# Kernel optimization log

Hardware: AMD Instinct MI355X
Metric: run time of the kernel (lower is better)

Reference implementation:

```python
import jax, jax.numpy as jnp
import numpy as np

T = 10          # time_steps
IN_DIM = 784    # 28*28
HID = 256
NCLS = 47
THRESH = 1.0
TAU_MEM = 2.0   # LIF membrane time constant
TAU_OUT = 2.0   # readout EMA time constant


@jax.custom_vjp
def spike_fn(u):
    # Heaviside spike on (v - threshold), surrogate gradient in bwd.
    return (u >= 0.0).astype(u.dtype)

def _spike_fwd(u):
    return spike_fn(u), u

def _spike_bwd(u, g):
    # sigmoid surrogate derivative, slope 4
    s = jax.nn.sigmoid(4.0 * u)
    return (g * 4.0 * s * (1.0 - s),)

spike_fn.defvjp(_spike_fwd, _spike_bwd)


def setup_inputs() -> dict:
    key = jax.random.key(0)
    k1, k2, k3 = jax.random.split(key, 3)
    x = jax.random.uniform(k1, (4096, 1, 28, 28), dtype=jnp.float32)
    W1 = jax.random.normal(k2, (IN_DIM, HID), dtype=jnp.float32) / np.float32(np.sqrt(IN_DIM))
    b1 = jnp.zeros((HID,), jnp.float32)
    Wr = jax.random.normal(k3, (HID, NCLS), dtype=jnp.float32) / np.float32(np.sqrt(HID))
    br = jnp.zeros((NCLS,), jnp.float32)
    return {"x": x, "W1": W1, "b1": b1, "Wr": Wr, "br": br}


def reference(x, W1, b1, Wr, br):
    B = x.shape[0]
    xf = x.reshape(B, -1)  # [B, 784] pixel intensities in [0,1]
    # rate_encode_flat: Bernoulli(p=pixel) spikes per timestep -> [T, B, 784]
    ek = jax.random.key(42)
    seq = (jax.random.uniform(ek, (T, B, IN_DIM), dtype=xf.dtype) < xf[None]).astype(xf.dtype)

    def step(carry, s_t):
        v_hid, v_out = carry
        I_hid = s_t @ W1 + b1                      # [B, HID]
        v_hid = v_hid + (I_hid - v_hid) / TAU_MEM  # leaky integration
        spk = spike_fn(v_hid - THRESH)             # spike emission
        v_hid = v_hid * (1.0 - spk)                # hard reset to 0
        I = spk @ Wr + br                          # [B, NCLS]
        v_out = v_out + (I - v_out) / TAU_OUT      # output EMA
        return (v_hid, v_out), None

    init = (jnp.zeros((B, HID), xf.dtype), jnp.zeros((B, NCLS), xf.dtype))
    (_, v_out), _ = jax.lax.scan(step, init, seq)
    return v_out
```

## Files before the change

### kernel.cpp

```cpp
#include <hip/hip_runtime.h>
#include <stdint.h>


#define T_STEPS 10
#define BATCH   4096
#define IN_DIM  784
#define HID     256
#define NCLS    47
#define NROWS   (T_STEPS * BATCH)
#define KWORDS  25
#define KPAD    800
#define M_TILE  160

#define WS_W1HI_OFF 46039040u
#define WS_W1MD_OFF (46039040u + 409600u)
#define WS_W1LO_OFF (46039040u + 819200u)

typedef __attribute__((ext_vector_type(8))) short    bf16x8;
typedef __attribute__((ext_vector_type(4))) float    f32x4;
typedef __attribute__((ext_vector_type(4))) uint32_t u32x4;

__device__ __forceinline__ uint32_t rotl32(uint32_t x, uint32_t r) {
    return __builtin_amdgcn_alignbit(x, x, 32u - r);
}

__device__ __forceinline__ uint32_t tf_hash(uint32_t lo) {
    const uint32_t ks1 = 42u;
    const uint32_t ks2 = 0x1BD11BDAu ^ 42u;
    uint32_t x0 = 0u;
    uint32_t x1 = lo + ks1;
#define TF_RND(r) { x0 += x1; x1 = rotl32(x1, r); x1 ^= x0; }
    TF_RND(13) TF_RND(15) TF_RND(26) TF_RND(6)
    x0 += ks1; x1 += ks2 + 1u;
    TF_RND(17) TF_RND(29) TF_RND(16) TF_RND(24)
    x0 += ks2; x1 += 2u;
    TF_RND(13) TF_RND(15) TF_RND(26) TF_RND(6)
    x1 += ks1 + 3u;
    TF_RND(17) TF_RND(29) TF_RND(16) TF_RND(24)
    x0 += ks1; x1 += ks2 + 4u;
    TF_RND(13) TF_RND(15) TF_RND(26) TF_RND(6)
    x0 += ks2; x1 += 5u;
#undef TF_RND
    return x0 ^ x1;
}

__device__ __forceinline__ uint32_t hash2(uint32_t ib, const float* xp) {
    float2 xx = *(const float2*)xp;
    uint32_t w = 0u;
    w |= ((float)(tf_hash(ib + 0u) >> 9) < xx.x * 8388608.0f) ? 0x3F80u : 0u;
    w |= ((float)(tf_hash(ib + 1u) >> 9) < xx.y * 8388608.0f) ? 0x3F800000u : 0u;
    return w;
}

__global__ __launch_bounds__(256) void splitk_k(
        const float* __restrict__ W1, ushort* __restrict__ hiT,
        ushort* __restrict__ midT, ushort* __restrict__ loT) {
    int n = blockIdx.x;
    for (int k = threadIdx.x; k < KPAD; k += 256) {
        float w = (k < IN_DIM) ? W1[k * HID + n] : 0.0f;
        uint32_t u = __float_as_uint(w);
        uint32_t hb = (u + 0x7FFFu + ((u >> 16) & 1u)) >> 16;
        float hf = __uint_as_float(hb << 16);
        float r1 = w - hf;
        uint32_t u1 = __float_as_uint(r1);
        uint32_t mb = (u1 + 0x7FFFu + ((u1 >> 16) & 1u)) >> 16;
        float mf2 = __uint_as_float(mb << 16);
        float r2 = r1 - mf2;
        uint32_t u2 = __float_as_uint(r2);
        uint32_t lb = (u2 + 0x7FFFu + ((u2 >> 16) & 1u)) >> 16;
        hiT [n * KPAD + k] = (ushort)hb;
        midT[n * KPAD + k] = (ushort)mb;
        loT [n * KPAD + k] = (ushort)lb;
    }
}

#define LDS_B0  20480
#define B_BUFSZ 49152
#define A_BUFSZ 10240
#define I0_LDW  258
#define G_LDW   260
#define G_OFF   83200

__global__ __launch_bounds__(512, 1) void fused_gemm_k(
        const ushort* __restrict__ hiT, const ushort* __restrict__ midT,
        const ushort* __restrict__ loT, const float* __restrict__ b1,
        const float* __restrict__ x, const float* __restrict__ Wr,
        const float* __restrict__ br, float* __restrict__ out) {
    __shared__ __align__(16) char lds[118784];

    const int tid = threadIdx.x;
    const int l   = tid & 63;
    const int wv  = tid >> 6;
    const int wm  = wv >> 2;
    const int wn  = wv & 3;
    const int b0  = blockIdx.x << 4;

    f32x4 acc[5][4] = {};

    const int q   = l >> 4;
    const int sig = q ^ (l & 3) ^ ((l >> 2) & 3);
    const int a_rd = wm * 5120 + ((l & 15) << 6) + (sig << 4);
    const int b_rd = (((wn << 6) + (l & 15)) << 6) + (sig << 4);

    const ushort* hi_p[2];
    const ushort* md_p[2];
    const ushort* lo_p[2];
    int bdst[2];
#pragma unroll
    for (int i = 0; i < 2; ++i) {
        int s  = (i << 9) + tid;
        int n  = s >> 2;
        int qs = s & 3;
        int qd = qs ^ (n & 3) ^ ((n >> 2) & 3);
        size_t eoff = (size_t)n * KPAD + ((size_t)qd << 3);
        hi_p[i] = hiT  + eoff;
        md_p[i] = midT + eoff;
        lo_p[i] = loT  + eoff;
        bdst[i] = ((i << 9) + (wv << 6)) << 4;
    }

    int      adst[5];
    const float* txp[5];
    uint32_t tib[5];
    int      tpp[5];
#pragma unroll
    for (int s = 0; s < 5; ++s) {
        int tau = tid + (s << 9);
        int row = tau >> 4;
        int p   = tau & 15;
        int qd  = (p >> 2) ^ (row & 3) ^ ((row >> 2) & 3);
        adst[s] = (row << 6) + (qd << 4) + ((p & 3) << 2);
        int rowg = ((row >> 4) * BATCH) + b0 + (row & 15);
        txp[s]  = x + (size_t)(b0 + (row & 15)) * IN_DIM + (p << 1);
        tib[s]  = (uint32_t)rowg * (uint32_t)IN_DIM + (uint32_t)(p << 1);
        tpp[s]  = p;
    }

#define STAGE_B(koff, bbase) \
    _Pragma("unroll") \
    for (int i = 0; i < 2; ++i) { \
        __builtin_amdgcn_global_load_lds( \
            (const __attribute__((address_space(1))) void*)(hi_p[i] + (koff)), \
            (__attribute__((address_space(3))) void*)(lds + (bbase) + bdst[i]), \
            16, 0, 0); \
        __builtin_amdgcn_global_load_lds( \
            (const __attribute__((address_space(1))) void*)(md_p[i] + (koff)), \
            (__attribute__((address_space(3))) void*)(lds + (bbase) + 16384 + bdst[i]), \
            16, 0, 0); \
        __builtin_amdgcn_global_load_lds( \
            (const __attribute__((address_space(1))) void*)(lo_p[i] + (koff)), \
            (__attribute__((address_space(3))) void*)(lds + (bbase) + 32768 + bdst[i]), \
            16, 0, 0); \
    }

#define HASH_TASK(s, koff, abase, is_tail) { \
    uint32_t w_ = 0u; \
    if (!(is_tail) || tpp[s] < 8) \
        w_ = hash2(tib[s] + (uint32_t)(koff), txp[s] + (koff)); \
    *(uint32_t*)(lds + (abase) + adst[s]) = w_; }

#define MFMA_CHUNK(s) \
    _Pragma("unroll") \
    for (int m = (s) * 12; m < (s) * 12 + 12; ++m) { \
        const int nt_ = m / 15, r_ = m % 15, pl_ = r_ / 5, mt_ = r_ % 5; \
        acc[mt_][nt_] = __builtin_amdgcn_mfma_f32_16x16x32_bf16( \
            af[mt_], bfr[pl_][nt_], acc[mt_][nt_], 0, 0, 0); \
    }

#define PRELOAD_FRAGS(bufidx) \
    const char* A = lds + (bufidx) * A_BUFSZ; \
    const char* B = lds + LDS_B0 + (bufidx) * B_BUFSZ; \
    bf16x8 af[5]; \
    bf16x8 bfr[3][4]; \
    _Pragma("unroll") \
    for (int mt = 0; mt < 5; ++mt) \
        af[mt] = *(const bf16x8*)(A + a_rd + (mt << 10)); \
    _Pragma("unroll") \
    for (int nt = 0; nt < 4; ++nt) { \
        bfr[0][nt] = *(const bf16x8*)(B + b_rd + (nt << 10)); \
        bfr[1][nt] = *(const bf16x8*)(B + 16384 + b_rd + (nt << 10)); \
        bfr[2][nt] = *(const bf16x8*)(B + 32768 + b_rd + (nt << 10)); \
    }

    STAGE_B(0, LDS_B0)
    HASH_TASK(0, 0, 0, false)
    HASH_TASK(1, 0, 0, false)
    HASH_TASK(2, 0, 0, false)
    HASH_TASK(3, 0, 0, false)
    HASH_TASK(4, 0, 0, false)
    __syncthreads();

    int cur = 0;
#pragma unroll 1
    for (int kw = 0; kw < KWORDS - 1; ++kw) {
        const int  nxt  = cur ^ 1;
        const int  koff = (kw + 1) << 5;
        const bool tail = (kw == KWORDS - 2);

        STAGE_B(koff, LDS_B0 + nxt * B_BUFSZ)
        PRELOAD_FRAGS(cur)

        const int ab = nxt * A_BUFSZ;
        HASH_TASK(0, koff, ab, tail)  MFMA_CHUNK(0)
        HASH_TASK(1, koff, ab, tail)  MFMA_CHUNK(1)
        HASH_TASK(2, koff, ab, tail)  MFMA_CHUNK(2)
        HASH_TASK(3, koff, ab, tail)  MFMA_CHUNK(3)
        HASH_TASK(4, koff, ab, tail)  MFMA_CHUNK(4)

        __syncthreads();
        cur = nxt;
    }

    {
        PRELOAD_FRAGS(cur)
        MFMA_CHUNK(0) MFMA_CHUNK(1) MFMA_CHUNK(2) MFMA_CHUNK(3) MFMA_CHUNK(4)
    }
#undef STAGE_B
#undef HASH_TASK
#undef MFMA_CHUNK
#undef PRELOAD_FRAGS

    const int c0 = l & 15;
    float b1v[4];
#pragma unroll
    for (int nt = 0; nt < 4; ++nt)
        b1v[nt] = b1[(wn << 6) + (nt << 4) + c0];

    __syncthreads();
    float* i0   = (float*)lds;
    float* gbuf = (float*)(lds + G_OFF);

    if (wm == 0) {
#pragma unroll
        for (int mt = 0; mt < 5; ++mt)
#pragma unroll
            for (int nt = 0; nt < 4; ++nt) {
                int col = (wn << 6) + (nt << 4) + c0;
#pragma unroll
                for (int r = 0; r < 4; ++r) {
                    int j = (q << 2) + r;
                    i0[(mt * 16 + j) * I0_LDW + col] = acc[mt][nt][r] + b1v[nt];
                }
            }
    }
    __syncthreads();

    if (wm == 1) {
#pragma unroll
        for (int nt = 0; nt < 4; ++nt) {
            int col = (wn << 6) + (nt << 4) + c0;
#pragma unroll
            for (int r = 0; r < 4; ++r) {
                int j = (q << 2) + r;
                float v = 0.f, ga = 0.f, wt = 0.0009765625f;
#pragma unroll
                for (int t = 0; t < 5; ++t) {
                    float I = i0[(t * 16 + j) * I0_LDW + col];
                    v = v + (I - v) * 0.5f;
                    if (v >= 1.0f) { ga += wt; v = 0.f; }
                    wt += wt;
                }
#pragma unroll
                for (int mt = 0; mt < 5; ++mt) {
                    float I = acc[mt][nt][r] + b1v[nt];
                    v = v + (I - v) * 0.5f;
                    if (v >= 1.0f) { ga += wt; v = 0.f; }
                    wt += wt;
                }
                gbuf[j * G_LDW + col] = ga;
            }
        }
    }
    __syncthreads();

    {
        const int c = l;
        if (c < NCLS) {
            float brv = br[c] * 0.9990234375f;
#pragma unroll
            for (int rr = 0; rr < 2; ++rr) {
                int j = (wv << 1) + rr;
                const float* gb = &gbuf[j * G_LDW];
                float a = 0.f;
                for (int h4 = 0; h4 < 64; ++h4) {
                    float w0 = Wr[((h4 << 2) + 0) * NCLS + c];
                    float w1 = Wr[((h4 << 2) + 1) * NCLS + c];
                    float w2 = Wr[((h4 << 2) + 2) * NCLS + c];
                    float w3 = Wr[((h4 << 2) + 3) * NCLS + c];
                    float4 gg = *(const float4*)&gb[h4 << 2];
                    a = fmaf(gg.x, w0, a);
                    a = fmaf(gg.y, w1, a);
                    a = fmaf(gg.z, w2, a);
                    a = fmaf(gg.w, w3, a);
                }
                out[(b0 + j) * NCLS + c] = a + brv;
            }
        }
    }
}

extern "C" void kernel_launch(void* const* d_in, const int* in_sizes, int n_in,
                              void* d_out, int out_size, void* d_ws, size_t ws_size,
                              hipStream_t stream) {
    const float* x  = (const float*)d_in[0];
    const float* W1 = (const float*)d_in[1];
    const float* b1 = (const float*)d_in[2];
    const float* Wr = (const float*)d_in[3];
    const float* br = (const float*)d_in[4];
    float* out = (float*)d_out;

    ushort* w1hi  = (ushort*)((char*)d_ws + WS_W1HI_OFF);
    ushort* w1md  = (ushort*)((char*)d_ws + WS_W1MD_OFF);
    ushort* w1lo  = (ushort*)((char*)d_ws + WS_W1LO_OFF);

    splitk_k<<<HID, 256, 0, stream>>>(W1, w1hi, w1md, w1lo);
    fused_gemm_k<<<BATCH / 16, 512, 0, stream>>>(w1hi, w1md, w1lo, b1, x,
                                                 Wr, br, out);
}
```

Measured before the change: 171.8 us.

## Halve batch tile per block, single-buffer B, and raise occupancy to four blocks

Result: slower. 176.7 us (+2.9%).

```diff
diff --git a/kernel.cpp b/kernel.cpp
--- a/kernel.cpp
+++ b/kernel.cpp
@@ -7,10 +7,8 @@
 #define IN_DIM  784
 #define HID     256
 #define NCLS    47
-#define NROWS   (T_STEPS * BATCH)
 #define KWORDS  25
 #define KPAD    800
-#define M_TILE  160
 
 #define WS_W1HI_OFF 46039040u
 #define WS_W1MD_OFF (46039040u + 409600u)
@@ -18,7 +16,6 @@
 
 typedef __attribute__((ext_vector_type(8))) short    bf16x8;
 typedef __attribute__((ext_vector_type(4))) float    f32x4;
-typedef __attribute__((ext_vector_type(4))) uint32_t u32x4;
 
 __device__ __forceinline__ uint32_t rotl32(uint32_t x, uint32_t r) {
     return __builtin_amdgcn_alignbit(x, x, 32u - r);
@@ -42,14 +39,6 @@
     x0 += ks2; x1 += 5u;
 #undef TF_RND
     return x0 ^ x1;
-}
-
-__device__ __forceinline__ uint32_t hash2(uint32_t ib, const float* xp) {
-    float2 xx = *(const float2*)xp;
-    uint32_t w = 0u;
-    w |= ((float)(tf_hash(ib + 0u) >> 9) < xx.x * 8388608.0f) ? 0x3F80u : 0u;
-    w |= ((float)(tf_hash(ib + 1u) >> 9) < xx.y * 8388608.0f) ? 0x3F800000u : 0u;
-    return w;
 }
 
 __global__ __launch_bounds__(256) void splitk_k(
@@ -74,33 +63,29 @@
     }
 }
 
-#define LDS_B0  20480
-#define B_BUFSZ 49152
-#define A_BUFSZ 10240
-#define I0_LDW  258
+#define A_BUFSZ 5120
+#define LDS_B0  10240
 #define G_LDW   260
-#define G_OFF   83200
-
-__global__ __launch_bounds__(512, 1) void fused_gemm_k(
+
+__global__ __launch_bounds__(512, 4) void fused_gemm_k(
         const ushort* __restrict__ hiT, const ushort* __restrict__ midT,
         const ushort* __restrict__ loT, const float* __restrict__ b1,
         const float* __restrict__ x, const float* __restrict__ Wr,
         const float* __restrict__ br, float* __restrict__ out) {
-    __shared__ __align__(16) char lds[118784];
+    __shared__ __align__(16) char lds[59392];
 
     const int tid = threadIdx.x;
     const int l   = tid & 63;
     const int wv  = tid >> 6;
-    const int wm  = wv >> 2;
-    const int wn  = wv & 3;
-    const int b0  = blockIdx.x << 4;
-
-    f32x4 acc[5][4] = {};
+    const int b0  = blockIdx.x << 3;
+
+    f32x4 acc[5][2] = {};
 
     const int q   = l >> 4;
+    const int c0  = l & 15;
     const int sig = q ^ (l & 3) ^ ((l >> 2) & 3);
-    const int a_rd = wm * 5120 + ((l & 15) << 6) + (sig << 4);
-    const int b_rd = (((wn << 6) + (l & 15)) << 6) + (sig << 4);
+    const int a_rd = (c0 << 6) + (sig << 4);
+    const int b_rd = (wv << 11) + (c0 << 6) + (sig << 4);
 
     const ushort* hi_p[2];
     const ushort* md_p[2];
@@ -119,182 +104,173 @@
         bdst[i] = ((i << 9) + (wv << 6)) << 4;
     }
 
+    const int eL = tid & 31;
     int      adst[5];
-    const float* txp[5];
+    int      xoff[5];
     uint32_t tib[5];
-    int      tpp[5];
 #pragma unroll
     for (int s = 0; s < 5; ++s) {
         int tau = tid + (s << 9);
-        int row = tau >> 4;
-        int p   = tau & 15;
+        int row = tau >> 5;
+        int p   = eL >> 1;
         int qd  = (p >> 2) ^ (row & 3) ^ ((row >> 2) & 3);
-        adst[s] = (row << 6) + (qd << 4) + ((p & 3) << 2);
-        int rowg = ((row >> 4) * BATCH) + b0 + (row & 15);
-        txp[s]  = x + (size_t)(b0 + (row & 15)) * IN_DIM + (p << 1);
-        tib[s]  = (uint32_t)rowg * (uint32_t)IN_DIM + (uint32_t)(p << 1);
-        tpp[s]  = p;
-    }
-
-#define STAGE_B(koff, bbase) \
+        adst[s] = (row << 6) + (qd << 4) + ((p & 3) << 2) + ((eL & 1) << 1);
+        int j   = row & 7;
+        int t   = row >> 3;
+        int rowg = t * BATCH + b0 + j;
+        xoff[s] = (b0 + j) * IN_DIM + eL;
+        tib[s]  = (uint32_t)rowg * (uint32_t)IN_DIM + (uint32_t)eL;
+    }
+
+#define STAGE_B(koff) \
     _Pragma("unroll") \
     for (int i = 0; i < 2; ++i) { \
         __builtin_amdgcn_global_load_lds( \
             (const __attribute__((address_space(1))) void*)(hi_p[i] + (koff)), \
-            (__attribute__((address_space(3))) void*)(lds + (bbase) + bdst[i]), \
+            (__attribute__((address_space(3))) void*)(lds + LDS_B0 + bdst[i]), \
             16, 0, 0); \
         __builtin_amdgcn_global_load_lds( \
             (const __attribute__((address_space(1))) void*)(md_p[i] + (koff)), \
-            (__attribute__((address_space(3))) void*)(lds + (bbase) + 16384 + bdst[i]), \
+            (__attribute__((address_space(3))) void*)(lds + LDS_B0 + 16384 + bdst[i]), \
             16, 0, 0); \
         __builtin_amdgcn_global_load_lds( \
             (const __attribute__((address_space(1))) void*)(lo_p[i] + (koff)), \
-            (__attribute__((address_space(3))) void*)(lds + (bbase) + 32768 + bdst[i]), \
+            (__attribute__((address_space(3))) void*)(lds + LDS_B0 + 32768 + bdst[i]), \
             16, 0, 0); \
     }
 
-#define HASH_TASK(s, koff, abase, is_tail) { \
-    uint32_t w_ = 0u; \
-    if (!(is_tail) || tpp[s] < 8) \
-        w_ = hash2(tib[s] + (uint32_t)(koff), txp[s] + (koff)); \
-    *(uint32_t*)(lds + (abase) + adst[s]) = w_; }
-
-#define MFMA_CHUNK(s) \
-    _Pragma("unroll") \
-    for (int m = (s) * 12; m < (s) * 12 + 12; ++m) { \
-        const int nt_ = m / 15, r_ = m % 15, pl_ = r_ / 5, mt_ = r_ % 5; \
-        acc[mt_][nt_] = __builtin_amdgcn_mfma_f32_16x16x32_bf16( \
-            af[mt_], bfr[pl_][nt_], acc[mt_][nt_], 0, 0, 0); \
+#define HASH_SLAB(koff, abase, is_tail) \
+    _Pragma("unroll") \
+    for (int s = 0; s < 5; ++s) { \
+        ushort w_ = 0; \
+        if (!(is_tail) || eL < 16) { \
+            float    xs = x[xoff[s] + (koff)] * 8388608.0f; \
+            uint32_t h  = tf_hash(tib[s] + (uint32_t)(koff)); \
+            if ((float)(h >> 9) < xs) w_ = (ushort)0x3F80; \
+        } \
+        *(ushort*)(lds + (abase) + adst[s]) = w_; \
     }
 
 #define PRELOAD_FRAGS(bufidx) \
     const char* A = lds + (bufidx) * A_BUFSZ; \
-    const char* B = lds + LDS_B0 + (bufidx) * B_BUFSZ; \
     bf16x8 af[5]; \
-    bf16x8 bfr[3][4]; \
+    bf16x8 bfr[3][2]; \
     _Pragma("unroll") \
     for (int mt = 0; mt < 5; ++mt) \
         af[mt] = *(const bf16x8*)(A + a_rd + (mt << 10)); \
     _Pragma("unroll") \
-    for (int nt = 0; nt < 4; ++nt) { \
-        bfr[0][nt] = *(const bf16x8*)(B + b_rd + (nt << 10)); \
-        bfr[1][nt] = *(const bf16x8*)(B + 16384 + b_rd + (nt << 10)); \
-        bfr[2][nt] = *(const bf16x8*)(B + 32768 + b_rd + (nt << 10)); \
-    }
-
-    STAGE_B(0, LDS_B0)
-    HASH_TASK(0, 0, 0, false)
-    HASH_TASK(1, 0, 0, false)
-    HASH_TASK(2, 0, 0, false)
-    HASH_TASK(3, 0, 0, false)
-    HASH_TASK(4, 0, 0, false)
+    for (int nt = 0; nt < 2; ++nt) { \
+        bfr[0][nt] = *(const bf16x8*)(lds + LDS_B0 + b_rd + (nt << 10)); \
+        bfr[1][nt] = *(const bf16x8*)(lds + LDS_B0 + 16384 + b_rd + (nt << 10)); \
+        bfr[2][nt] = *(const bf16x8*)(lds + LDS_B0 + 32768 + b_rd + (nt << 10)); \
+    }
+
+#define MFMA_ALL \
+    _Pragma("unroll") \
+    for (int nt = 0; nt < 2; ++nt) { \
+        _Pragma("unroll") \
+        for (int mt = 0; mt < 5; ++mt) { \
+            acc[mt][nt] = __builtin_amdgcn_mfma_f32_16x16x32_bf16(af[mt], bfr[0][nt], acc[mt][nt], 0, 0, 0); \
+            acc[mt][nt] = __builtin_amdgcn_mfma_f32_16x16x32_bf16(af[mt], bfr[1][nt], acc[mt][nt], 0, 0, 0); \
+            acc[mt][nt] = __builtin_amdgcn_mfma_f32_16x16x32_bf16(af[mt], bfr[2][nt], acc[mt][nt], 0, 0, 0); \
+        } \
+    }
+
+    STAGE_B(0)
+    HASH_SLAB(0, 0, false)
     __syncthreads();
 
     int cur = 0;
 #pragma unroll 1
-    for (int kw = 0; kw < KWORDS - 1; ++kw) {
-        const int  nxt  = cur ^ 1;
-        const int  koff = (kw + 1) << 5;
-        const bool tail = (kw == KWORDS - 2);
-
-        STAGE_B(koff, LDS_B0 + nxt * B_BUFSZ)
-        PRELOAD_FRAGS(cur)
-
-        const int ab = nxt * A_BUFSZ;
-        HASH_TASK(0, koff, ab, tail)  MFMA_CHUNK(0)
-        HASH_TASK(1, koff, ab, tail)  MFMA_CHUNK(1)
-        HASH_TASK(2, koff, ab, tail)  MFMA_CHUNK(2)
-        HASH_TASK(3, koff, ab, tail)  MFMA_CHUNK(3)
-        HASH_TASK(4, koff, ab, tail)  MFMA_CHUNK(4)
-
+    for (int kw = 0; kw < KWORDS; ++kw) {
+        {
+            PRELOAD_FRAGS(cur)
+            if (kw < KWORDS - 1) {
+                const int koff = (kw + 1) << 5;
+                if (kw == KWORDS - 2) { HASH_SLAB(koff, (cur ^ 1) * A_BUFSZ, true) }
+                else                  { HASH_SLAB(koff, (cur ^ 1) * A_BUFSZ, false) }
+            }
+            MFMA_ALL
+        }
         __syncthreads();
-        cur = nxt;
-    }
-
-    {
-        PRELOAD_FRAGS(cur)
-        MFMA_CHUNK(0) MFMA_CHUNK(1) MFMA_CHUNK(2) MFMA_CHUNK(3) MFMA_CHUNK(4)
+        if (kw < KWORDS - 1) {
+            STAGE_B((kw + 1) << 5)
+            __syncthreads();
+        }
+        cur ^= 1;
     }
 #undef STAGE_B
-#undef HASH_TASK
-#undef MFMA_CHUNK
+#undef HASH_SLAB
 #undef PRELOAD_FRAGS
-
-    const int c0 = l & 15;
-    float b1v[4];
-#pragma unroll
-    for (int nt = 0; nt < 4; ++nt)
-        b1v[nt] = b1[(wn << 6) + (nt << 4) + c0];
-
-    __syncthreads();
-    float* i0   = (float*)lds;
-    float* gbuf = (float*)(lds + G_OFF);
-
-    if (wm == 0) {
-#pragma unroll
-        for (int mt = 0; mt < 5; ++mt)
-#pragma unroll
-            for (int nt = 0; nt < 4; ++nt) {
-                int col = (wn << 6) + (nt << 4) + c0;
-#pragma unroll
-                for (int r = 0; r < 4; ++r) {
-                    int j = (q << 2) + r;
-                    i0[(mt * 16 + j) * I0_LDW + col] = acc[mt][nt][r] + b1v[nt];
-                }
-            }
-    }
-    __syncthreads();
-
-    if (wm == 1) {
-#pragma unroll
-        for (int nt = 0; nt < 4; ++nt) {
-            int col = (wn << 6) + (nt << 4) + c0;
-#pragma unroll
-            for (int r = 0; r < 4; ++r) {
-                int j = (q << 2) + r;
-                float v = 0.f, ga = 0.f, wt = 0.0009765625f;
-#pragma unroll
-                for (int t = 0; t < 5; ++t) {
-                    float I = i0[(t * 16 + j) * I0_LDW + col];
-                    v = v + (I - v) * 0.5f;
-                    if (v >= 1.0f) { ga += wt; v = 0.f; }
-                    wt += wt;
-                }
-#pragma unroll
-                for (int mt = 0; mt < 5; ++mt) {
-                    float I = acc[mt][nt][r] + b1v[nt];
-                    v = v + (I - v) * 0.5f;
-                    if (v >= 1.0f) { ga += wt; v = 0.f; }
-                    wt += wt;
-                }
-                gbuf[j * G_LDW + col] = ga;
-            }
-        }
+#undef MFMA_ALL
+
+    float b1v[2];
+#pragma unroll
+    for (int nt = 0; nt < 2; ++nt)
+        b1v[nt] = b1[(wv << 5) + (nt << 4) + c0];
+
+    float av[5][2][4];
+#pragma unroll
+    for (int mt = 0; mt < 5; ++mt)
+#pragma unroll
+        for (int nt = 0; nt < 2; ++nt)
+#pragma unroll
+            for (int rr = 0; rr < 4; ++rr)
+                av[mt][nt][rr] = acc[mt][nt][rr] + b1v[nt];
+
+    const int qh = q >> 1;
+    float g[2][4];
+#pragma unroll
+    for (int nt = 0; nt < 2; ++nt) {
+#pragma unroll
+        for (int rr = 0; rr < 4; ++rr) {
+            float v = 0.f, ga = 0.f, wt = 0.0009765625f;
+#pragma unroll
+            for (int m = 0; m < 5; ++m) {
+                float pv = __shfl_xor(av[m][nt][rr], 32);
+                float Ie = qh ? pv : av[m][nt][rr];
+                float Io = qh ? av[m][nt][rr] : pv;
+                v = v + (Ie - v) * 0.5f;
+                if (v >= 1.0f) { ga += wt; v = 0.f; }
+                wt += wt;
+                v = v + (Io - v) * 0.5f;
+                if (v >= 1.0f) { ga += wt; v = 0.f; }
+                wt += wt;
+            }
+            g[nt][rr] = ga;
+        }
+    }
+
+    float* gbuf = (float*)lds;
+    if (l < 32) {
+#pragma unroll
+        for (int nt = 0; nt < 2; ++nt)
+#pragma unroll
+            for (int rr = 0; rr < 4; ++rr) {
+                int j   = ((q & 1) << 2) + rr;
+                int col = (wv << 5) + (nt << 4) + c0;
+                gbuf[j * G_LDW + col] = g[nt][rr];
+            }
     }
     __syncthreads();
 
     {
         const int c = l;
         if (c < NCLS) {
-            float brv = br[c] * 0.9990234375f;
-#pragma unroll
-            for (int rr = 0; rr < 2; ++rr) {
-                int j = (wv << 1) + rr;
-                const float* gb = &gbuf[j * G_LDW];
-                float a = 0.f;
-                for (int h4 = 0; h4 < 64; ++h4) {
-                    float w0 = Wr[((h4 << 2) + 0) * NCLS + c];
-                    float w1 = Wr[((h4 << 2) + 1) * NCLS + c];
-                    float w2 = Wr[((h4 << 2) + 2) * NCLS + c];
-                    float w3 = Wr[((h4 << 2) + 3) * NCLS + c];
-                    float4 gg = *(const float4*)&gb[h4 << 2];
-                    a = fmaf(gg.x, w0, a);
-                    a = fmaf(gg.y, w1, a);
-                    a = fmaf(gg.z, w2, a);
-                    a = fmaf(gg.w, w3, a);
-                }
-                out[(b0 + j) * NCLS + c] = a + brv;
-            }
+            const float* gb = &gbuf[wv * G_LDW];
+            float a = 0.f;
+            for (int h4 = 0; h4 < 64; ++h4) {
+                float w0 = Wr[((h4 << 2) + 0) * NCLS + c];
+                float w1 = Wr[((h4 << 2) + 1) * NCLS + c];
+                float w2 = Wr[((h4 << 2) + 2) * NCLS + c];
+                float w3 = Wr[((h4 << 2) + 3) * NCLS + c];
+                float4 gg = *(const float4*)&gb[h4 << 2];
+                a = fmaf(gg.x, w0, a);
+                a = fmaf(gg.y, w1, a);
+                a = fmaf(gg.z, w2, a);
+                a = fmaf(gg.w, w3, a);
+            }
+            out[(b0 + wv) * NCLS + c] = a + br[c] * 0.9990234375f;
         }
     }
 }
@@ -314,6 +290,6 @@
     ushort* w1lo  = (ushort*)((char*)d_ws + WS_W1LO_OFF);
 
     splitk_k<<<HID, 256, 0, stream>>>(W1, w1hi, w1md, w1lo);
-    fused_gemm_k<<<BATCH / 16, 512, 0, stream>>>(w1hi, w1md, w1lo, b1, x,
-                                                 Wr, br, out);
-}
+    fused_gemm_k<<<BATCH / 8, 512, 0, stream>>>(w1hi, w1md, w1lo, b1, x,
+                                                Wr, br, out);
+}
```
